# Optimization experiments

Hardware: AMD Instinct MI355X
Metric: run time of the kernel (lower is better)

## Reference

```python
import jax, jax.numpy as jnp
import numpy as np

B, K = 512, 64
EBD, VFD = 256, 512
SENS = EBD + VFD            # 768 sensory inputs to layer 0
LAYERS = [512, 256, 64]     # inter, command, motor neurons (NCP wiring)


def _make_layer_params(key, in_features, hidden):
    ks = jax.random.split(key, 9)
    cat = in_features + hidden
    s = 1.0 / np.sqrt(cat)
    def lin(k):
        return jax.random.normal(k, (hidden, cat), dtype=jnp.float32) * s
    # sparsity mask: random NCP-style sparsity on the input block, dense recurrent block
    in_mask = (jax.random.uniform(ks[8], (hidden, in_features)) < 0.5).astype(jnp.float32)
    rec_mask = jnp.ones((hidden, hidden), dtype=jnp.float32)
    mask = jnp.concatenate([in_mask, rec_mask], axis=1)  # (hidden, in+hidden)
    return dict(
        ff1_w=lin(ks[0]), ff1_b=jnp.zeros((hidden,), jnp.float32),
        ff2_w=lin(ks[1]), ff2_b=jnp.zeros((hidden,), jnp.float32),
        ta_w=lin(ks[2]), ta_b=jnp.zeros((hidden,), jnp.float32),
        tb_w=lin(ks[3]), tb_b=jnp.zeros((hidden,), jnp.float32),
        mask=mask,
    )


def setup_inputs() -> dict:
    key = jax.random.key(0)
    k_base, k_vis, k0, k1, k2 = jax.random.split(key, 5)
    inp = {
        'base_expanded_seq': jax.random.normal(k_base, (B, K, EBD), dtype=jnp.float32),
        'visual_seq': jax.random.normal(k_vis, (B, K, VFD), dtype=jnp.float32),
    }
    in_feats = [SENS, LAYERS[0], LAYERS[1]]
    for li, (k, fin, hid) in enumerate(zip([k0, k1, k2], in_feats, LAYERS)):
        p = _make_layer_params(k, fin, hid)
        for name, v in p.items():
            inp[f'l{li}_{name}'] = v
    return inp


def _cfc_cell(x_in, h, ff1_w, ff1_b, ff2_w, ff2_b, ta_w, ta_b, tb_w, tb_b, mask, ts=1.0):
    # ncps CfCCell, mode='default', no backbone, sparsity mask on ff1/ff2
    x = jnp.concatenate([x_in, h], axis=-1)          # (B, in+hidden)
    ff1 = jnp.tanh(x @ (ff1_w * mask).T + ff1_b)
    ff2 = jnp.tanh(x @ (ff2_w * mask).T + ff2_b)
    t_a = x @ ta_w.T + ta_b
    t_b = x @ tb_w.T + tb_b
    t_interp = jax.nn.sigmoid(t_a * ts + t_b)
    return ff1 * (1.0 - t_interp) + t_interp * ff2


def reference(base_expanded_seq, visual_seq,
              l0_ff1_w, l0_ff1_b, l0_ff2_w, l0_ff2_b, l0_ta_w, l0_ta_b, l0_tb_w, l0_tb_b, l0_mask,
              l1_ff1_w, l1_ff1_b, l1_ff2_w, l1_ff2_b, l1_ta_w, l1_ta_b, l1_tb_w, l1_tb_b, l1_mask,
              l2_ff1_w, l2_ff1_b, l2_ff2_w, l2_ff2_b, l2_ta_w, l2_ta_b, l2_tb_w, l2_tb_b, l2_mask):
    layers = [
        (l0_ff1_w, l0_ff1_b, l0_ff2_w, l0_ff2_b, l0_ta_w, l0_ta_b, l0_tb_w, l0_tb_b, l0_mask),
        (l1_ff1_w, l1_ff1_b, l1_ff2_w, l1_ff2_b, l1_ta_w, l1_ta_b, l1_tb_w, l1_tb_b, l1_mask),
        (l2_ff1_w, l2_ff1_b, l2_ff2_w, l2_ff2_b, l2_ta_w, l2_ta_b, l2_tb_w, l2_tb_b, l2_mask),
    ]
    b = base_expanded_seq.shape[0]
    x_seq = jnp.concatenate([base_expanded_seq, visual_seq], axis=-1)  # (B,K,768)
    x_seq = jnp.swapaxes(x_seq, 0, 1)                                  # (K,B,768)
    h_init = tuple(jnp.zeros((b, h), dtype=x_seq.dtype) for h in LAYERS)

    def step(carry, x_t):
        inp = x_t
        new_hs = []
        for p, h in zip(layers, carry):
            h_new = _cfc_cell(inp, h, *p)
            inp = h_new
            new_hs.append(h_new)
        return tuple(new_hs), None

    final_h, _ = jax.lax.scan(step, h_init, x_seq)
    return final_h[-1]  # (B, motor_neurons) = last timestep motor-layer output
```

## Files before the change

### kernel.cpp

```cpp
#include <hip/hip_runtime.h>
#include <cmath>


typedef __attribute__((ext_vector_type(8))) _Float16 half8;
typedef __attribute__((ext_vector_type(4))) float f32x4;

#define DEVINL __device__ __forceinline__

struct Params {
  const float* base;
  const float* visual;
  const _Float16 *w0, *w1, *w2;
  const float *b0f1,*b0f2,*b0ta,*b0tb;
  const float *b1f1,*b1f2,*b1ta,*b1tb;
  const float *b2f1,*b2f2,*b2ta,*b2tb;
  _Float16 *xh0,*xl0,*xh1,*xl1;
  float *xacc0,*xacc1;
  _Float16 *h0h0,*h0h1,*h0l0,*h0l1;
  _Float16 *h1h0,*h1h1,*h1l0,*h1l1;
  _Float16 *h2h0,*h2h1,*h2l0,*h2l1;
  float* out;
};

DEVINL void gload(half8& d, const _Float16* a) {
  asm volatile("global_load_dwordx4 %0, %1, off" : "=v"(d) : "v"(a));
}
template <int V>
DEVINL void vmwait() {
  __builtin_amdgcn_s_waitcnt((V & 15) | (7 << 4) | (15 << 8) | ((V >> 4) << 14));
  __builtin_amdgcn_sched_barrier(0);
}

template <int C, int NC, int D, class AF>
DEVINL void pipe_iter(half8 (&buf)[D][6], f32x4 (&acc)[4], const AF& addr) {
  constexpr int issued = (C + D < NC) ? (C + D) : NC;
  vmwait<6 * (issued - C - 1)>();
  {
    half8 b0 = buf[C % D][0], b1 = buf[C % D][1];
    half8 b2 = buf[C % D][2], b3 = buf[C % D][3];
    half8 ah = buf[C % D][4], al = buf[C % D][5];
    acc[0] = __builtin_amdgcn_mfma_f32_16x16x32_f16(ah, b0, acc[0], 0, 0, 0);
    acc[0] = __builtin_amdgcn_mfma_f32_16x16x32_f16(al, b0, acc[0], 0, 0, 0);
    acc[1] = __builtin_amdgcn_mfma_f32_16x16x32_f16(ah, b1, acc[1], 0, 0, 0);
    acc[1] = __builtin_amdgcn_mfma_f32_16x16x32_f16(al, b1, acc[1], 0, 0, 0);
    acc[2] = __builtin_amdgcn_mfma_f32_16x16x32_f16(ah, b2, acc[2], 0, 0, 0);
    acc[2] = __builtin_amdgcn_mfma_f32_16x16x32_f16(al, b2, acc[2], 0, 0, 0);
    acc[3] = __builtin_amdgcn_mfma_f32_16x16x32_f16(ah, b3, acc[3], 0, 0, 0);
    acc[3] = __builtin_amdgcn_mfma_f32_16x16x32_f16(al, b3, acc[3], 0, 0, 0);
  }
  if constexpr (C + D < NC) {
#pragma unroll
    for (int j = 0; j < 6; ++j) gload(buf[C % D][j], addr(C + D, j));
  }
  if constexpr (C + 1 < NC) pipe_iter<C + 1, NC, D>(buf, acc, addr);
}

template <int NC, class AF>
DEVINL void gemm_pipe(f32x4 (&acc)[4], const AF& addr) {
  constexpr int D = (NC < 4) ? NC : 4;
  half8 buf[D][6];
#pragma unroll
  for (int c = 0; c < D; ++c)
#pragma unroll
    for (int j = 0; j < 6; ++j) gload(buf[c][j], addr(c, j));
  pipe_iter<0, NC, D>(buf, acc, addr);
}

DEVINL void run_xprep(const Params& p, int t, int b ) {
  _Float16* xh = (t & 1) ? p.xh1 : p.xh0;
  _Float16* xl = (t & 1) ? p.xl1 : p.xl0;
  int tid = b * 256 + threadIdx.x;
#pragma unroll
  for (int i = tid; i < 49152; i += 12288) {
    int m = i / 96;
    int k = (i - m * 96) * 8;
    const float* src = (k < 256) ? (p.base + (m * 64 + t) * 256 + k)
                                 : (p.visual + (m * 64 + t) * 512 + (k - 256));
    const f32x4* q = (const f32x4*)src;
    f32x4 v0 = q[0], v1 = q[1];
    half8 hh, ll;
#pragma unroll
    for (int j = 0; j < 4; ++j) {
      _Float16 a = (_Float16)v0[j]; hh[j] = a;     ll[j]     = (_Float16)(v0[j] - (float)a);
      _Float16 c = (_Float16)v1[j]; hh[j + 4] = c; ll[j + 4] = (_Float16)(v1[j] - (float)c);
    }
    int off = (((m >> 4) * 24 + (k >> 5)) * 64 + ((k >> 3) & 3) * 16 + (m & 15)) * 8;
    *(half8*)(xh + off) = hh;
    *(half8*)(xl + off) = ll;
  }
}

DEVINL void run_xgemm(const Params& p, int t, int b ) {
  const _Float16* xh = (t & 1) ? p.xh1 : p.xh0;
  const _Float16* xl = (t & 1) ? p.xl1 : p.xl0;
  float* xacc = (t & 1) ? p.xacc1 : p.xacc0;
  const int lane = threadIdx.x & 63, wv = threadIdx.x >> 6;
  const int lr = lane & 15, lq = lane >> 4;
  const int mt = b >> 5, nt = b & 31;
  const int m_base = mt * 64 + wv * 16, n0 = nt * 16;
  const int mt16 = mt * 4 + wv;

  f32x4 acc[4];
#pragma unroll
  for (int g = 0; g < 4; ++g) acc[g] = f32x4{0.f, 0.f, 0.f, 0.f};

  const _Float16* wpk = p.w0 + (nt * 40) * 512 + lane * 8;
  const _Float16* apk = xh + (mt16 * 24) * 512 + lane * 8;
  const _Float16* lpk = xl + (mt16 * 24) * 512 + lane * 8;
  auto addr = [&](int c, int j) -> const _Float16* {
    if (j < 4) return wpk + (j * (32 * 40) + c) * 512;
    return ((j == 4) ? apk : lpk) + c * 512;
  };
  gemm_pipe<24>(acc, addr);

  const int n = n0 + lr;
  const int mrow = m_base + lq * 4;
#pragma unroll
  for (int g = 0; g < 4; ++g)
#pragma unroll
    for (int r = 0; r < 4; ++r)
      xacc[(mrow + r) * 2048 + g * 512 + n] = acc[g][r];
}

template <int L>
DEVINL void run_rec(const Params& p, int t, int b) {
  constexpr int HH = (L == 0) ? 512 : ((L == 1) ? 256 : 64);
  constexpr int NC = (L == 0) ? 16 : ((L == 1) ? 24 : 10);
  constexpr int NCH = HH / 32;

  const int lane = threadIdx.x & 63, wv = threadIdx.x >> 6;
  const int lr = lane & 15, lq = lane >> 4;
  int mt, nt;
  if constexpr (L == 0)      { mt = b >> 5; nt = b & 31; }
  else if constexpr (L == 1) { mt = b >> 4; nt = b & 15; }
  else                       { mt = b >> 2; nt = b & 3; }
  const int m_base = mt * 64 + wv * 16, n0 = nt * 16;
  const int mt16 = mt * 4 + wv;
  const int wbuf = t & 1;

  const _Float16 *hph, *hpl, *pah = nullptr, *pal = nullptr;
  _Float16 *oh, *ol;
  const float *bf1p, *bf2p, *btap, *btbp;
  const _Float16* wpk;
  if constexpr (L == 0) {
    wpk = p.w0 + (nt * 40) * 512 + lane * 8;
    hph = wbuf ? p.h0h0 : p.h0h1;  hpl = wbuf ? p.h0l0 : p.h0l1;
    oh  = wbuf ? p.h0h1 : p.h0h0;  ol  = wbuf ? p.h0l1 : p.h0l0;
    bf1p = p.b0f1; bf2p = p.b0f2; btap = p.b0ta; btbp = p.b0tb;
  } else if constexpr (L == 1) {
    wpk = p.w1 + (nt * 24) * 512 + lane * 8;
    pah = wbuf ? p.h0h1 : p.h0h0;  pal = wbuf ? p.h0l1 : p.h0l0;
    hph = wbuf ? p.h1h0 : p.h1h1;  hpl = wbuf ? p.h1l0 : p.h1l1;
    oh  = wbuf ? p.h1h1 : p.h1h0;  ol  = wbuf ? p.h1l1 : p.h1l0;
    bf1p = p.b1f1; bf2p = p.b1f2; btap = p.b1ta; btbp = p.b1tb;
  } else {
    wpk = p.w2 + (nt * 10) * 512 + lane * 8;
    pah = wbuf ? p.h1h1 : p.h1h0;  pal = wbuf ? p.h1l1 : p.h1l0;
    hph = wbuf ? p.h2h0 : p.h2h1;  hpl = wbuf ? p.h2l0 : p.h2l1;
    oh  = wbuf ? p.h2h1 : p.h2h0;  ol  = wbuf ? p.h2l1 : p.h2l0;
    bf1p = p.b2f1; bf2p = p.b2f2; btap = p.b2ta; btbp = p.b2tb;
  }

  f32x4 acc[4];
#pragma unroll
  for (int g = 0; g < 4; ++g) acc[g] = f32x4{0.f, 0.f, 0.f, 0.f};

  const int lane8 = lane * 8;
  auto addr = [&](int c, int j) -> const _Float16* {
    if constexpr (L == 0) {
      if (j < 4) return wpk + (j * (32 * 40) + 24 + c) * 512;
      return ((j == 4) ? hph : hpl) + (mt16 * 16 + c) * 512 + lane8;
    } else if constexpr (L == 1) {
      if (j < 4) return wpk + (j * (16 * 24) + c) * 512;
      if (c < 16) return ((j == 4) ? pah : pal) + (mt16 * 16 + c) * 512 + lane8;
      return ((j == 4) ? hph : hpl) + (mt16 * 8 + (c - 16)) * 512 + lane8;
    } else {
      if (j < 4) return wpk + (j * (4 * 10) + c) * 512;
      if (c < 8) return ((j == 4) ? pah : pal) + (mt16 * 8 + c) * 512 + lane8;
      return ((j == 4) ? hph : hpl) + (mt16 * 2 + (c - 8)) * 512 + lane8;
    }
  };
  gemm_pipe<NC>(acc, addr);

  const float* xacc = nullptr;
  if constexpr (L == 0) xacc = (t & 1) ? p.xacc1 : p.xacc0;

  const int n = n0 + lr;
  const float bff1 = bf1p[n], bff2 = bf2p[n], bta = btap[n], btb = btbp[n];
  const int obase = ((m_base >> 4) * NCH + (n >> 5)) * 512 + ((n >> 3) & 3) * 128 + (n & 7);
#pragma unroll
  for (int r = 0; r < 4; ++r) {
    const int row = m_base + lq * 4 + r;
    const int lrr = lq * 4 + r;
    float a0 = acc[0][r], a1 = acc[1][r], a2 = acc[2][r], a3 = acc[3][r];
    if constexpr (L == 0) {
      const float* xb = xacc + row * 2048 + n;
      a0 += xb[0]; a1 += xb[512]; a2 += xb[1024]; a3 += xb[1536];
    }
    float vf1 = a0 + bff1;
    float vf2 = a1 + bff2;
    float vt  = (a2 + bta) + (a3 + btb);
    float ff1 = tanhf(vf1);
    float ff2 = tanhf(vf2);
    float ti  = 1.0f / (1.0f + __expf(-vt));
    float hv  = ff1 + ti * (ff2 - ff1);
    _Float16 hh = (_Float16)hv;
    oh[obase + lrr * 8] = hh;
    ol[obase + lrr * 8] = (_Float16)(hv - (float)hh);
    if constexpr (L == 2) {
      if (t == 63) p.out[row * 64 + n] = hv;
    }
  }
}

__global__ __launch_bounds__(256, 2) void cfc_step(Params p, int s) {
  const int bid = blockIdx.x;
  if (bid < 48)       { int t = s + 2; if (t >= 0 && t < 64) run_xprep(p, t, bid); }
  else if (bid < 304) { int t = s + 1; if (t >= 0 && t < 64) run_xgemm(p, t, bid - 48); }
  else if (bid < 560) { int t = s;     if (t >= 0 && t < 64) run_rec<0>(p, t, bid - 304); }
  else if (bid < 688) { int t = s - 1; if (t >= 0 && t < 64) run_rec<1>(p, t, bid - 560); }
  else                { int t = s - 2; if (t >= 0 && t < 64) run_rec<2>(p, t, bid - 688); }
}

__global__ void prep_w_pk(const float* __restrict__ w, const float* __restrict__ mask,
                          _Float16* __restrict__ dst, int WK, int total) {
  int i = blockIdx.x * 256 + threadIdx.x;
  if (i >= total) return;
  int e = i & 7, lane = (i >> 3) & 63, rem = i >> 9;
  int NCk = WK >> 5;
  int c = rem % NCk, nt = rem / NCk;
  int n = nt * 16 + (lane & 15);
  int k = c * 32 + (lane >> 4) * 8 + e;
  float v = w[n * WK + k];
  if (mask) v *= mask[n * WK + k];
  dst[i] = (_Float16)v;
}

__global__ void zero_kernel(unsigned* __restrict__ p, int n) {
  int i = blockIdx.x * 256 + threadIdx.x;
  if (i < n) p[i] = 0u;
}

extern "C" void kernel_launch(void* const* d_in, const int* in_sizes, int n_in,
                              void* d_out, int out_size, void* d_ws, size_t ws_size,
                              hipStream_t stream) {
  _Float16* w0  = (_Float16*)d_ws;
  _Float16* w1  = w0 + 2621440;
  _Float16* w2  = w1 + 786432;
  _Float16* xh0 = w2 + 81920;
  _Float16* xl0 = xh0 + 393216;
  _Float16* xh1 = xl0 + 393216;
  _Float16* xl1 = xh1 + 393216;
  _Float16* hb  = xl1 + 393216;
  _Float16* h0h0 = hb;            _Float16* h0h1 = h0h0 + 262144;
  _Float16* h0l0 = h0h1 + 262144; _Float16* h0l1 = h0l0 + 262144;
  _Float16* h1h0 = h0l1 + 262144; _Float16* h1h1 = h1h0 + 131072;
  _Float16* h1l0 = h1h1 + 131072; _Float16* h1l1 = h1l0 + 131072;
  _Float16* h2h0 = h1l1 + 131072; _Float16* h2h1 = h2h0 + 32768;
  _Float16* h2l0 = h2h1 + 32768;  _Float16* h2l1 = h2l0 + 32768;
  float* xacc0 = (float*)(h2l1 + 32768);
  float* xacc1 = xacc0 + 1048576;

  const int h_uints = 1703936 / 2;
  zero_kernel<<<(h_uints + 255) / 256, 256, 0, stream>>>((unsigned*)hb, h_uints);

  const float* F = nullptr;
  auto in = [&](int i) { return (const float*)d_in[i]; };

  prep_w_pk<<<2560, 256, 0, stream>>>(in(2),  in(10), w0 + 0 * 655360, 1280, 655360);
  prep_w_pk<<<2560, 256, 0, stream>>>(in(4),  in(10), w0 + 1 * 655360, 1280, 655360);
  prep_w_pk<<<2560, 256, 0, stream>>>(in(6),  F,      w0 + 2 * 655360, 1280, 655360);
  prep_w_pk<<<2560, 256, 0, stream>>>(in(8),  F,      w0 + 3 * 655360, 1280, 655360);
  prep_w_pk<<<768,  256, 0, stream>>>(in(11), in(19), w1 + 0 * 196608, 768,  196608);
  prep_w_pk<<<768,  256, 0, stream>>>(in(13), in(19), w1 + 1 * 196608, 768,  196608);
  prep_w_pk<<<768,  256, 0, stream>>>(in(15), F,      w1 + 2 * 196608, 768,  196608);
  prep_w_pk<<<768,  256, 0, stream>>>(in(17), F,      w1 + 3 * 196608, 768,  196608);
  prep_w_pk<<<80,   256, 0, stream>>>(in(20), in(28), w2 + 0 * 20480,  320,  20480);
  prep_w_pk<<<80,   256, 0, stream>>>(in(22), in(28), w2 + 1 * 20480,  320,  20480);
  prep_w_pk<<<80,   256, 0, stream>>>(in(24), F,      w2 + 2 * 20480,  320,  20480);
  prep_w_pk<<<80,   256, 0, stream>>>(in(26), F,      w2 + 3 * 20480,  320,  20480);

  Params p;
  p.base = in(0); p.visual = in(1);
  p.w0 = w0; p.w1 = w1; p.w2 = w2;
  p.b0f1 = in(3);  p.b0f2 = in(5);  p.b0ta = in(7);  p.b0tb = in(9);
  p.b1f1 = in(12); p.b1f2 = in(14); p.b1ta = in(16); p.b1tb = in(18);
  p.b2f1 = in(21); p.b2f2 = in(23); p.b2ta = in(25); p.b2tb = in(27);
  p.xh0 = xh0; p.xl0 = xl0; p.xh1 = xh1; p.xl1 = xl1;
  p.xacc0 = xacc0; p.xacc1 = xacc1;
  p.h0h0 = h0h0; p.h0h1 = h0h1; p.h0l0 = h0l0; p.h0l1 = h0l1;
  p.h1h0 = h1h0; p.h1h1 = h1h1; p.h1l0 = h1l0; p.h1l1 = h1l1;
  p.h2h0 = h2h0; p.h2h1 = h2h1; p.h2l0 = h2l0; p.h2l1 = h2l1;
  p.out = (float*)d_out;

  for (int s = -2; s < 66; ++s) {
    cfc_step<<<720, 256, 0, stream>>>(p, s);
  }
}
```

Before: 1.237 ms.

## Compute two N-tiles per block to reuse activation loads across MFMAs

Each GEMM block (x-projection and all three recurrent layers) now computes two 16-wide output column tiles instead of one. Each activation hi/lo fragment is loaded once and reused across eight weight fragments rather than four, and the grid shrinks from 720 to 384 blocks. The goal is to cut redundant activation loads and per-block launch and epilogue overhead. In exchange each block uses more registers for buffers and accumulators, and with half as many blocks per step the GPU has less parallelism to hide latency.

```diff
diff --git a/kernel.cpp b/kernel.cpp
--- a/kernel.cpp
+++ b/kernel.cpp
@@ -31,39 +31,27 @@
   __builtin_amdgcn_sched_barrier(0);
 }
 
-template <int C, int NC, int D, class AF>
-DEVINL void pipe_iter(half8 (&buf)[D][6], f32x4 (&acc)[4], const AF& addr) {
+template <int C, int NC, int D, int J, class AF, class MF>
+DEVINL void pipe_iter(half8 (&buf)[D][J], const AF& addr, const MF& mf) {
   constexpr int issued = (C + D < NC) ? (C + D) : NC;
-  vmwait<6 * (issued - C - 1)>();
-  {
-    half8 b0 = buf[C % D][0], b1 = buf[C % D][1];
-    half8 b2 = buf[C % D][2], b3 = buf[C % D][3];
-    half8 ah = buf[C % D][4], al = buf[C % D][5];
-    acc[0] = __builtin_amdgcn_mfma_f32_16x16x32_f16(ah, b0, acc[0], 0, 0, 0);
-    acc[0] = __builtin_amdgcn_mfma_f32_16x16x32_f16(al, b0, acc[0], 0, 0, 0);
-    acc[1] = __builtin_amdgcn_mfma_f32_16x16x32_f16(ah, b1, acc[1], 0, 0, 0);
-    acc[1] = __builtin_amdgcn_mfma_f32_16x16x32_f16(al, b1, acc[1], 0, 0, 0);
-    acc[2] = __builtin_amdgcn_mfma_f32_16x16x32_f16(ah, b2, acc[2], 0, 0, 0);
-    acc[2] = __builtin_amdgcn_mfma_f32_16x16x32_f16(al, b2, acc[2], 0, 0, 0);
-    acc[3] = __builtin_amdgcn_mfma_f32_16x16x32_f16(ah, b3, acc[3], 0, 0, 0);
-    acc[3] = __builtin_amdgcn_mfma_f32_16x16x32_f16(al, b3, acc[3], 0, 0, 0);
-  }
+  vmwait<J * (issued - C - 1)>();
+  mf(buf[C % D]);
   if constexpr (C + D < NC) {
 #pragma unroll
-    for (int j = 0; j < 6; ++j) gload(buf[C % D][j], addr(C + D, j));
-  }
-  if constexpr (C + 1 < NC) pipe_iter<C + 1, NC, D>(buf, acc, addr);
-}
-
-template <int NC, class AF>
-DEVINL void gemm_pipe(f32x4 (&acc)[4], const AF& addr) {
+    for (int j = 0; j < J; ++j) gload(buf[C % D][j], addr(C + D, j));
+  }
+  if constexpr (C + 1 < NC) pipe_iter<C + 1, NC, D, J>(buf, addr, mf);
+}
+
+template <int NC, int J, class AF, class MF>
+DEVINL void gemm_pipe(const AF& addr, const MF& mf) {
   constexpr int D = (NC < 4) ? NC : 4;
-  half8 buf[D][6];
+  half8 buf[D][J];
 #pragma unroll
   for (int c = 0; c < D; ++c)
 #pragma unroll
-    for (int j = 0; j < 6; ++j) gload(buf[c][j], addr(c, j));
-  pipe_iter<0, NC, D>(buf, acc, addr);
+    for (int j = 0; j < J; ++j) gload(buf[c][j], addr(c, j));
+  pipe_iter<0, NC, D, J>(buf, addr, mf);
 }
 
 DEVINL void run_xprep(const Params& p, int t, int b ) {
@@ -96,30 +84,46 @@
   float* xacc = (t & 1) ? p.xacc1 : p.xacc0;
   const int lane = threadIdx.x & 63, wv = threadIdx.x >> 6;
   const int lr = lane & 15, lq = lane >> 4;
-  const int mt = b >> 5, nt = b & 31;
-  const int m_base = mt * 64 + wv * 16, n0 = nt * 16;
-  const int mt16 = mt * 4 + wv;
-
-  f32x4 acc[4];
-#pragma unroll
-  for (int g = 0; g < 4; ++g) acc[g] = f32x4{0.f, 0.f, 0.f, 0.f};
-
-  const _Float16* wpk = p.w0 + (nt * 40) * 512 + lane * 8;
+  const int mt = b >> 4, nt2 = b & 15;
+  const int m_base = mt * 64 + wv * 16;
+  const int mt16 = mt * 4 + wv, ntA = nt2 * 2;
+
+  f32x4 acc[2][4];
+#pragma unroll
+  for (int u = 0; u < 2; ++u)
+#pragma unroll
+    for (int g = 0; g < 4; ++g) acc[u][g] = f32x4{0.f, 0.f, 0.f, 0.f};
+
+  const _Float16* wpk = p.w0 + (ntA * 40) * 512 + lane * 8;
   const _Float16* apk = xh + (mt16 * 24) * 512 + lane * 8;
   const _Float16* lpk = xl + (mt16 * 24) * 512 + lane * 8;
   auto addr = [&](int c, int j) -> const _Float16* {
-    if (j < 4) return wpk + (j * (32 * 40) + c) * 512;
-    return ((j == 4) ? apk : lpk) + c * 512;
+    if (j < 8) { int u = j >> 2, g = j & 3;
+      return wpk + u * 20480 + (g * 1280 + c) * 512; }
+    return ((j == 8) ? apk : lpk) + c * 512;
   };
-  gemm_pipe<24>(acc, addr);
-
-  const int n = n0 + lr;
+  auto mf = [&](half8 (&B)[10]) {
+    half8 ah = B[8], al = B[9];
+#pragma unroll
+    for (int u = 0; u < 2; ++u)
+#pragma unroll
+      for (int g = 0; g < 4; ++g) {
+        acc[u][g] = __builtin_amdgcn_mfma_f32_16x16x32_f16(ah, B[u * 4 + g], acc[u][g], 0, 0, 0);
+        acc[u][g] = __builtin_amdgcn_mfma_f32_16x16x32_f16(al, B[u * 4 + g], acc[u][g], 0, 0, 0);
+      }
+  };
+  gemm_pipe<24, 10>(addr, mf);
+
   const int mrow = m_base + lq * 4;
 #pragma unroll
-  for (int g = 0; g < 4; ++g)
-#pragma unroll
-    for (int r = 0; r < 4; ++r)
-      xacc[(mrow + r) * 2048 + g * 512 + n] = acc[g][r];
+  for (int u = 0; u < 2; ++u) {
+    const int n = (ntA + u) * 16 + lr;
+#pragma unroll
+    for (int g = 0; g < 4; ++g)
+#pragma unroll
+      for (int r = 0; r < 4; ++r)
+        xacc[(mrow + r) * 2048 + g * 512 + n] = acc[u][g][r];
+  }
 }
 
 template <int L>
@@ -127,15 +131,18 @@
   constexpr int HH = (L == 0) ? 512 : ((L == 1) ? 256 : 64);
   constexpr int NC = (L == 0) ? 16 : ((L == 1) ? 24 : 10);
   constexpr int NCH = HH / 32;
+  constexpr int NTS = (L == 0) ? 40 : ((L == 1) ? 24 : 10);
+  constexpr int GP  = (L == 0) ? 1280 : ((L == 1) ? 384 : 40);
+  constexpr int CB  = (L == 0) ? 24 : 0;
 
   const int lane = threadIdx.x & 63, wv = threadIdx.x >> 6;
   const int lr = lane & 15, lq = lane >> 4;
-  int mt, nt;
-  if constexpr (L == 0)      { mt = b >> 5; nt = b & 31; }
-  else if constexpr (L == 1) { mt = b >> 4; nt = b & 15; }
-  else                       { mt = b >> 2; nt = b & 3; }
-  const int m_base = mt * 64 + wv * 16, n0 = nt * 16;
-  const int mt16 = mt * 4 + wv;
+  int mt, nt2;
+  if constexpr (L == 0)      { mt = b >> 4; nt2 = b & 15; }
+  else if constexpr (L == 1) { mt = b >> 3; nt2 = b & 7; }
+  else                       { mt = b >> 1; nt2 = b & 1; }
+  const int m_base = mt * 64 + wv * 16;
+  const int mt16 = mt * 4 + wv, ntA = nt2 * 2;
   const int wbuf = t & 1;
 
   const _Float16 *hph, *hpl, *pah = nullptr, *pal = nullptr;
@@ -143,72 +150,87 @@
   const float *bf1p, *bf2p, *btap, *btbp;
   const _Float16* wpk;
   if constexpr (L == 0) {
-    wpk = p.w0 + (nt * 40) * 512 + lane * 8;
+    wpk = p.w0 + (ntA * NTS) * 512 + lane * 8;
     hph = wbuf ? p.h0h0 : p.h0h1;  hpl = wbuf ? p.h0l0 : p.h0l1;
     oh  = wbuf ? p.h0h1 : p.h0h0;  ol  = wbuf ? p.h0l1 : p.h0l0;
     bf1p = p.b0f1; bf2p = p.b0f2; btap = p.b0ta; btbp = p.b0tb;
   } else if constexpr (L == 1) {
-    wpk = p.w1 + (nt * 24) * 512 + lane * 8;
+    wpk = p.w1 + (ntA * NTS) * 512 + lane * 8;
     pah = wbuf ? p.h0h1 : p.h0h0;  pal = wbuf ? p.h0l1 : p.h0l0;
     hph = wbuf ? p.h1h0 : p.h1h1;  hpl = wbuf ? p.h1l0 : p.h1l1;
     oh  = wbuf ? p.h1h1 : p.h1h0;  ol  = wbuf ? p.h1l1 : p.h1l0;
     bf1p = p.b1f1; bf2p = p.b1f2; btap = p.b1ta; btbp = p.b1tb;
   } else {
-    wpk = p.w2 + (nt * 10) * 512 + lane * 8;
+    wpk = p.w2 + (ntA * NTS) * 512 + lane * 8;
     pah = wbuf ? p.h1h1 : p.h1h0;  pal = wbuf ? p.h1l1 : p.h1l0;
     hph = wbuf ? p.h2h0 : p.h2h1;  hpl = wbuf ? p.h2l0 : p.h2l1;
     oh  = wbuf ? p.h2h1 : p.h2h0;  ol  = wbuf ? p.h2l1 : p.h2l0;
     bf1p = p.b2f1; bf2p = p.b2f2; btap = p.b2ta; btbp = p.b2tb;
   }
 
-  f32x4 acc[4];
-#pragma unroll
-  for (int g = 0; g < 4; ++g) acc[g] = f32x4{0.f, 0.f, 0.f, 0.f};
+  f32x4 acc[2][4];
+#pragma unroll
+  for (int u = 0; u < 2; ++u)
+#pragma unroll
+    for (int g = 0; g < 4; ++g) acc[u][g] = f32x4{0.f, 0.f, 0.f, 0.f};
 
   const int lane8 = lane * 8;
   auto addr = [&](int c, int j) -> const _Float16* {
+    if (j < 8) { int u = j >> 2, g = j & 3;
+      return wpk + u * (NTS * 512) + (g * GP + CB + c) * 512; }
+    const bool hi = (j == 8);
     if constexpr (L == 0) {
-      if (j < 4) return wpk + (j * (32 * 40) + 24 + c) * 512;
-      return ((j == 4) ? hph : hpl) + (mt16 * 16 + c) * 512 + lane8;
+      return (hi ? hph : hpl) + (mt16 * 16 + c) * 512 + lane8;
     } else if constexpr (L == 1) {
-      if (j < 4) return wpk + (j * (16 * 24) + c) * 512;
-      if (c < 16) return ((j == 4) ? pah : pal) + (mt16 * 16 + c) * 512 + lane8;
-      return ((j == 4) ? hph : hpl) + (mt16 * 8 + (c - 16)) * 512 + lane8;
+      if (c < 16) return (hi ? pah : pal) + (mt16 * 16 + c) * 512 + lane8;
+      return (hi ? hph : hpl) + (mt16 * 8 + (c - 16)) * 512 + lane8;
     } else {
-      if (j < 4) return wpk + (j * (4 * 10) + c) * 512;
-      if (c < 8) return ((j == 4) ? pah : pal) + (mt16 * 8 + c) * 512 + lane8;
-      return ((j == 4) ? hph : hpl) + (mt16 * 2 + (c - 8)) * 512 + lane8;
+      if (c < 8) return (hi ? pah : pal) + (mt16 * 8 + c) * 512 + lane8;
+      return (hi ? hph : hpl) + (mt16 * 2 + (c - 8)) * 512 + lane8;
     }
   };
-  gemm_pipe<NC>(acc, addr);
+  auto mf = [&](half8 (&B)[10]) {
+    half8 ah = B[8], al = B[9];
+#pragma unroll
+    for (int u = 0; u < 2; ++u)
+#pragma unroll
+      for (int g = 0; g < 4; ++g) {
+        acc[u][g] = __builtin_amdgcn_mfma_f32_16x16x32_f16(ah, B[u * 4 + g], acc[u][g], 0, 0, 0);
+        acc[u][g] = __builtin_amdgcn_mfma_f32_16x16x32_f16(al, B[u * 4 + g], acc[u][g], 0, 0, 0);
+      }
+  };
+  gemm_pipe<NC, 10>(addr, mf);
 
   const float* xacc = nullptr;
   if constexpr (L == 0) xacc = (t & 1) ? p.xacc1 : p.xacc0;
 
-  const int n = n0 + lr;
-  const float bff1 = bf1p[n], bff2 = bf2p[n], bta = btap[n], btb = btbp[n];
-  const int obase = ((m_base >> 4) * NCH + (n >> 5)) * 512 + ((n >> 3) & 3) * 128 + (n & 7);
-#pragma unroll
-  for (int r = 0; r < 4; ++r) {
-    const int row = m_base + lq * 4 + r;
-    const int lrr = lq * 4 + r;
-    float a0 = acc[0][r], a1 = acc[1][r], a2 = acc[2][r], a3 = acc[3][r];
-    if constexpr (L == 0) {
-      const float* xb = xacc + row * 2048 + n;
-      a0 += xb[0]; a1 += xb[512]; a2 += xb[1024]; a3 += xb[1536];
-    }
-    float vf1 = a0 + bff1;
-    float vf2 = a1 + bff2;
-    float vt  = (a2 + bta) + (a3 + btb);
-    float ff1 = tanhf(vf1);
-    float ff2 = tanhf(vf2);
-    float ti  = 1.0f / (1.0f + __expf(-vt));
-    float hv  = ff1 + ti * (ff2 - ff1);
-    _Float16 hh = (_Float16)hv;
-    oh[obase + lrr * 8] = hh;
-    ol[obase + lrr * 8] = (_Float16)(hv - (float)hh);
-    if constexpr (L == 2) {
-      if (t == 63) p.out[row * 64 + n] = hv;
+#pragma unroll
+  for (int u = 0; u < 2; ++u) {
+    const int n = (ntA + u) * 16 + lr;
+    const float bff1 = bf1p[n], bff2 = bf2p[n], bta = btap[n], btb = btbp[n];
+    const int obase = (mt16 * NCH + (n >> 5)) * 512 + ((n >> 3) & 3) * 128 + (n & 7);
+#pragma unroll
+    for (int r = 0; r < 4; ++r) {
+      const int row = m_base + lq * 4 + r;
+      const int lrr = lq * 4 + r;
+      float a0 = acc[u][0][r], a1 = acc[u][1][r], a2 = acc[u][2][r], a3 = acc[u][3][r];
+      if constexpr (L == 0) {
+        const float* xb = xacc + row * 2048 + n;
+        a0 += xb[0]; a1 += xb[512]; a2 += xb[1024]; a3 += xb[1536];
+      }
+      float vf1 = a0 + bff1;
+      float vf2 = a1 + bff2;
+      float vt  = (a2 + bta) + (a3 + btb);
+      float ff1 = tanhf(vf1);
+      float ff2 = tanhf(vf2);
+      float ti  = 1.0f / (1.0f + __expf(-vt));
+      float hv  = ff1 + ti * (ff2 - ff1);
+      _Float16 hh = (_Float16)hv;
+      oh[obase + lrr * 8] = hh;
+      ol[obase + lrr * 8] = (_Float16)(hv - (float)hh);
+      if constexpr (L == 2) {
+        if (t == 63) p.out[row * 64 + n] = hv;
+      }
     }
   }
 }
@@ -216,10 +238,10 @@
 __global__ __launch_bounds__(256, 2) void cfc_step(Params p, int s) {
   const int bid = blockIdx.x;
   if (bid < 48)       { int t = s + 2; if (t >= 0 && t < 64) run_xprep(p, t, bid); }
-  else if (bid < 304) { int t = s + 1; if (t >= 0 && t < 64) run_xgemm(p, t, bid - 48); }
-  else if (bid < 560) { int t = s;     if (t >= 0 && t < 64) run_rec<0>(p, t, bid - 304); }
-  else if (bid < 688) { int t = s - 1; if (t >= 0 && t < 64) run_rec<1>(p, t, bid - 560); }
-  else                { int t = s - 2; if (t >= 0 && t < 64) run_rec<2>(p, t, bid - 688); }
+  else if (bid < 176) { int t = s + 1; if (t >= 0 && t < 64) run_xgemm(p, t, bid - 48); }
+  else if (bid < 304) { int t = s;     if (t >= 0 && t < 64) run_rec<0>(p, t, bid - 176); }
+  else if (bid < 368) { int t = s - 1; if (t >= 0 && t < 64) run_rec<1>(p, t, bid - 304); }
+  else                { int t = s - 2; if (t >= 0 && t < 64) run_rec<2>(p, t, bid - 368); }
 }
 
 __global__ void prep_w_pk(const float* __restrict__ w, const float* __restrict__ mask,
@@ -294,6 +316,6 @@
   p.out = (float*)d_out;
 
   for (int s = -2; s < 66; ++s) {
-    cfc_step<<<720, 256, 0, stream>>>(p, s);
-  }
-}
+    cfc_step<<<384, 256, 0, stream>>>(p, s);
+  }
+}
```

Result: slower. 1.429 ms (+15.5%).

## Fuse layer-0 input GEMM into recurrent GEMM, drop xacc staging

Applied to the files above, without the earlier changes.

Removes the separate input-projection GEMM stage that wrote fp32 partial sums to a staging buffer. Layer-0 recurrent blocks now run one 40-chunk GEMM over both the converted input and the hidden state, which shortens the software pipeline by one stage and cuts the grid from 720 to 464 blocks. It also removes the fp32 staging write and read. In exchange, the input-projection work now sits on the critical path of each layer-0 block, which makes those blocks longer.

```diff
diff --git a/kernel.cpp b/kernel.cpp
--- a/kernel.cpp
+++ b/kernel.cpp
@@ -15,7 +15,6 @@
   const float *b1f1,*b1f2,*b1ta,*b1tb;
   const float *b2f1,*b2f2,*b2ta,*b2tb;
   _Float16 *xh0,*xl0,*xh1,*xl1;
-  float *xacc0,*xacc1;
   _Float16 *h0h0,*h0h1,*h0l0,*h0l1;
   _Float16 *h1h0,*h1h1,*h1l0,*h1l1;
   _Float16 *h2h0,*h2h1,*h2l0,*h2l1;
@@ -90,42 +89,10 @@
   }
 }
 
-DEVINL void run_xgemm(const Params& p, int t, int b ) {
-  const _Float16* xh = (t & 1) ? p.xh1 : p.xh0;
-  const _Float16* xl = (t & 1) ? p.xl1 : p.xl0;
-  float* xacc = (t & 1) ? p.xacc1 : p.xacc0;
-  const int lane = threadIdx.x & 63, wv = threadIdx.x >> 6;
-  const int lr = lane & 15, lq = lane >> 4;
-  const int mt = b >> 5, nt = b & 31;
-  const int m_base = mt * 64 + wv * 16, n0 = nt * 16;
-  const int mt16 = mt * 4 + wv;
-
-  f32x4 acc[4];
-#pragma unroll
-  for (int g = 0; g < 4; ++g) acc[g] = f32x4{0.f, 0.f, 0.f, 0.f};
-
-  const _Float16* wpk = p.w0 + (nt * 40) * 512 + lane * 8;
-  const _Float16* apk = xh + (mt16 * 24) * 512 + lane * 8;
-  const _Float16* lpk = xl + (mt16 * 24) * 512 + lane * 8;
-  auto addr = [&](int c, int j) -> const _Float16* {
-    if (j < 4) return wpk + (j * (32 * 40) + c) * 512;
-    return ((j == 4) ? apk : lpk) + c * 512;
-  };
-  gemm_pipe<24>(acc, addr);
-
-  const int n = n0 + lr;
-  const int mrow = m_base + lq * 4;
-#pragma unroll
-  for (int g = 0; g < 4; ++g)
-#pragma unroll
-    for (int r = 0; r < 4; ++r)
-      xacc[(mrow + r) * 2048 + g * 512 + n] = acc[g][r];
-}
-
 template <int L>
 DEVINL void run_rec(const Params& p, int t, int b) {
   constexpr int HH = (L == 0) ? 512 : ((L == 1) ? 256 : 64);
-  constexpr int NC = (L == 0) ? 16 : ((L == 1) ? 24 : 10);
+  constexpr int NC = (L == 0) ? 40 : ((L == 1) ? 24 : 10);
   constexpr int NCH = HH / 32;
 
   const int lane = threadIdx.x & 63, wv = threadIdx.x >> 6;
@@ -144,6 +111,7 @@
   const _Float16* wpk;
   if constexpr (L == 0) {
     wpk = p.w0 + (nt * 40) * 512 + lane * 8;
+    pah = wbuf ? p.xh1 : p.xh0;    pal = wbuf ? p.xl1 : p.xl0;
     hph = wbuf ? p.h0h0 : p.h0h1;  hpl = wbuf ? p.h0l0 : p.h0l1;
     oh  = wbuf ? p.h0h1 : p.h0h0;  ol  = wbuf ? p.h0l1 : p.h0l0;
     bf1p = p.b0f1; bf2p = p.b0f2; btap = p.b0ta; btbp = p.b0tb;
@@ -168,8 +136,9 @@
   const int lane8 = lane * 8;
   auto addr = [&](int c, int j) -> const _Float16* {
     if constexpr (L == 0) {
-      if (j < 4) return wpk + (j * (32 * 40) + 24 + c) * 512;
-      return ((j == 4) ? hph : hpl) + (mt16 * 16 + c) * 512 + lane8;
+      if (j < 4) return wpk + (j * (32 * 40) + c) * 512;
+      if (c < 24) return ((j == 4) ? pah : pal) + (mt16 * 24 + c) * 512 + lane8;
+      return ((j == 4) ? hph : hpl) + (mt16 * 16 + (c - 24)) * 512 + lane8;
     } else if constexpr (L == 1) {
       if (j < 4) return wpk + (j * (16 * 24) + c) * 512;
       if (c < 16) return ((j == 4) ? pah : pal) + (mt16 * 16 + c) * 512 + lane8;
@@ -182,9 +151,6 @@
   };
   gemm_pipe<NC>(acc, addr);
 
-  const float* xacc = nullptr;
-  if constexpr (L == 0) xacc = (t & 1) ? p.xacc1 : p.xacc0;
-
   const int n = n0 + lr;
   const float bff1 = bf1p[n], bff2 = bf2p[n], bta = btap[n], btb = btbp[n];
   const int obase = ((m_base >> 4) * NCH + (n >> 5)) * 512 + ((n >> 3) & 3) * 128 + (n & 7);
@@ -193,10 +159,6 @@
     const int row = m_base + lq * 4 + r;
     const int lrr = lq * 4 + r;
     float a0 = acc[0][r], a1 = acc[1][r], a2 = acc[2][r], a3 = acc[3][r];
-    if constexpr (L == 0) {
-      const float* xb = xacc + row * 2048 + n;
-      a0 += xb[0]; a1 += xb[512]; a2 += xb[1024]; a3 += xb[1536];
-    }
     float vf1 = a0 + bff1;
     float vf2 = a1 + bff2;
     float vt  = (a2 + bta) + (a3 + btb);
@@ -215,11 +177,10 @@
 
 __global__ __launch_bounds__(256, 2) void cfc_step(Params p, int s) {
   const int bid = blockIdx.x;
-  if (bid < 48)       { int t = s + 2; if (t >= 0 && t < 64) run_xprep(p, t, bid); }
-  else if (bid < 304) { int t = s + 1; if (t >= 0 && t < 64) run_xgemm(p, t, bid - 48); }
-  else if (bid < 560) { int t = s;     if (t >= 0 && t < 64) run_rec<0>(p, t, bid - 304); }
-  else if (bid < 688) { int t = s - 1; if (t >= 0 && t < 64) run_rec<1>(p, t, bid - 560); }
-  else                { int t = s - 2; if (t >= 0 && t < 64) run_rec<2>(p, t, bid - 688); }
+  if (bid < 48)       { int t = s + 1; if (t >= 0 && t < 64) run_xprep(p, t, bid); }
+  else if (bid < 304) { int t = s;     if (t >= 0 && t < 64) run_rec<0>(p, t, bid - 48); }
+  else if (bid < 432) { int t = s - 1; if (t >= 0 && t < 64) run_rec<1>(p, t, bid - 304); }
+  else                { int t = s - 2; if (t >= 0 && t < 64) run_rec<2>(p, t, bid - 432); }
 }
 
 __global__ void prep_w_pk(const float* __restrict__ w, const float* __restrict__ mask,
@@ -258,8 +219,6 @@
   _Float16* h1l0 = h1h1 + 131072; _Float16* h1l1 = h1l0 + 131072;
   _Float16* h2h0 = h1l1 + 131072; _Float16* h2h1 = h2h0 + 32768;
   _Float16* h2l0 = h2h1 + 32768;  _Float16* h2l1 = h2l0 + 32768;
-  float* xacc0 = (float*)(h2l1 + 32768);
-  float* xacc1 = xacc0 + 1048576;
 
   const int h_uints = 1703936 / 2;
   zero_kernel<<<(h_uints + 255) / 256, 256, 0, stream>>>((unsigned*)hb, h_uints);
@@ -287,13 +246,12 @@
   p.b1f1 = in(12); p.b1f2 = in(14); p.b1ta = in(16); p.b1tb = in(18);
   p.b2f1 = in(21); p.b2f2 = in(23); p.b2ta = in(25); p.b2tb = in(27);
   p.xh0 = xh0; p.xl0 = xl0; p.xh1 = xh1; p.xl1 = xl1;
-  p.xacc0 = xacc0; p.xacc1 = xacc1;
   p.h0h0 = h0h0; p.h0h1 = h0h1; p.h0l0 = h0l0; p.h0l1 = h0l1;
   p.h1h0 = h1h0; p.h1h1 = h1h1; p.h1l0 = h1l0; p.h1l1 = h1l1;
   p.h2h0 = h2h0; p.h2h1 = h2h1; p.h2l0 = h2l0; p.h2l1 = h2l1;
   p.out = (float*)d_out;
 
-  for (int s = -2; s < 66; ++s) {
-    cfc_step<<<720, 256, 0, stream>>>(p, s);
-  }
-}
+  for (int s = -1; s < 66; ++s) {
+    cfc_step<<<464, 256, 0, stream>>>(p, s);
+  }
+}
```

After: 1.162 ms. -6.0%, faster.
